# Optimization experiments

Measured on AMD Instinct MI355X. Metric: run time of the kernel, lower is better.

The kernel has to match this reference:

```python
import jax, jax.numpy as jnp
import numpy as np

N_NODES = 10000
N_EDGES = 160000
D_IN = 512
D_OUT = 512


def setup_inputs() -> dict:
    key = jax.random.key(0)
    k_x, k_e, k_wl, k_wr = jax.random.split(key, 4)
    x = jax.random.normal(k_x, (N_NODES, D_IN), dtype=jnp.float32)
    edge_index = jax.random.randint(k_e, (2, N_EDGES), 0, N_NODES, dtype=jnp.int64)
    scale = 1.0 / np.sqrt(D_IN)
    W_l = jax.random.normal(k_wl, (D_IN, D_OUT), dtype=jnp.float32) * scale
    W_r = jax.random.normal(k_wr, (D_IN, D_OUT), dtype=jnp.float32) * scale
    b = jnp.zeros((D_OUT,), dtype=jnp.float32)
    return {"x": x, "edge_index": edge_index, "W_l": W_l, "W_r": W_r, "b": b}


def reference(x, edge_index, W_l, W_r, b):
    # dropout p=0.0 -> identity
    src = edge_index[0]  # message sources (x_j)
    dst = edge_index[1]  # aggregation targets (i)
    n = x.shape[0]
    # mean neighbor aggregation: scatter-add messages, divide by in-degree
    msg = x[src]                                   # [E, D_in]
    agg = jax.ops.segment_sum(msg, dst, num_segments=n)        # [N, D_in]
    deg = jax.ops.segment_sum(jnp.ones((src.shape[0],), x.dtype), dst, num_segments=n)
    mean = agg / jnp.maximum(deg, 1.0)[:, None]
    # SAGEConv: lin_l(aggregated) + lin_r(root), bias in lin_l
    h = mean @ W_l + b + x @ W_r                   # [N, D_out]
    # Swish activation
    return h * jax.nn.sigmoid(h)
```

## Files before the change

kernel.cpp:

```cpp
#include <hip/hip_runtime.h>
#include <cstdint>
#include <cstddef>

typedef unsigned short ushort_t;
typedef __attribute__((ext_vector_type(8))) short short8;
typedef __attribute__((ext_vector_type(4))) float float4_;
typedef __attribute__((ext_vector_type(2))) float float2_;

#define GLOBAL_AS __attribute__((address_space(1)))
#define LDS_AS    __attribute__((address_space(3)))

#define D_FEAT 512
#define KDIM   1024
#define CAP    80
#define BK     128

__device__ __forceinline__ ushort_t f2bf(float f) {
    union { float f; unsigned int i; } v; v.f = f;
    unsigned int x = v.i;
    unsigned int r = (x + 0x7fffu + ((x >> 16) & 1u)) >> 16;
    return (ushort_t)r;
}

__device__ __forceinline__ void accq(float* acc, uint2 v) {
    float2_ a01 = __builtin_amdgcn_cvt_pk_f32_fp8(v.x, false);
    float2_ a23 = __builtin_amdgcn_cvt_pk_f32_fp8(v.x, true);
    float2_ a45 = __builtin_amdgcn_cvt_pk_f32_fp8(v.y, false);
    float2_ a67 = __builtin_amdgcn_cvt_pk_f32_fp8(v.y, true);
    acc[0] += a01.x; acc[1] += a01.y;
    acc[2] += a23.x; acc[3] += a23.y;
    acc[4] += a45.x; acc[5] += a45.y;
    acc[6] += a67.x; acc[7] += a67.y;
}

__global__ __launch_bounds__(256) void prep_kernel(
    const float* __restrict__ Wl, const float* __restrict__ Wr,
    const float* __restrict__ x, const int* __restrict__ ei,
    ushort_t* __restrict__ BT, ushort_t* __restrict__ xb,
    unsigned char* __restrict__ xq, unsigned int* __restrict__ cnt,
    int* __restrict__ colbuf, int N, int E, int nchunks, int cb) {
    int b = blockIdx.x;
    int t = threadIdx.x;
    if (b < cb) {
        int idx = b * 256 + t;
        if (idx >= nchunks) return;
        int row = idx >> 7;
        int c = (idx & 127) << 2;
        float4 v = *(const float4*)&x[(size_t)row * D_FEAT + c];
        ushort_t o[4] = {f2bf(v.x), f2bf(v.y), f2bf(v.z), f2bf(v.w)};
        *(uint2*)&xb[(size_t)row * D_FEAT + c] = *(const uint2*)o;
        int pk = 0;
        pk = __builtin_amdgcn_cvt_pk_fp8_f32(v.x, v.y, pk, false);
        pk = __builtin_amdgcn_cvt_pk_fp8_f32(v.z, v.w, pk, true);
        *(int*)&xq[(size_t)row * D_FEAT + c] = pk;
    } else if (b < cb + 128) {
        int bb = b - cb;
        __shared__ float tile[64][68];
        int kb = (bb & 15) * 64, nb = (bb >> 4) * 64;
#pragma unroll
        for (int ph = 0; ph < 4; ++ph) {
            int f = t * 4 + ph * 1024;
            int k = f >> 6, n = f & 63;
            int gk = kb + k;
            const float* W = (gk < 512) ? (Wl + (size_t)gk * 512 + nb + n)
                                        : (Wr + (size_t)(gk - 512) * 512 + nb + n);
            *(float4*)&tile[k][n] = *(const float4*)W;
        }
        __syncthreads();
#pragma unroll
        for (int ph = 0; ph < 4; ++ph) {
            int f = t * 4 + ph * 1024;
            int n = f >> 6, k = f & 63;
            ushort_t tmp[4];
#pragma unroll
            for (int j = 0; j < 4; ++j) tmp[j] = f2bf(tile[k + j][n]);
            *(uint2*)&BT[(size_t)(nb + n) * KDIM + kb + k] = *(const uint2*)tmp;
        }
    } else {
        int e = ((b - cb - 128) * 256 + t) * 2;
        if (e >= E) return;
        unsigned int V = cnt[N];
        int2 d2 = *(const int2*)&ei[E + e];
        int2 s2 = *(const int2*)&ei[e];
        unsigned int p0 = atomicAdd(&cnt[d2.x], 1u) - V;
        if (p0 < CAP) colbuf[(size_t)d2.x * CAP + p0] = s2.x;
        if (e + 1 < E) {
            unsigned int p1 = atomicAdd(&cnt[d2.y], 1u) - V;
            if (p1 < CAP) colbuf[(size_t)d2.y * CAP + p1] = s2.y;
        }
    }
}

__global__ __launch_bounds__(256) void agg_kernel(
    const unsigned char* __restrict__ xq, ushort_t* __restrict__ mb,
    const unsigned int* __restrict__ cnt, const int* __restrict__ colbuf,
    int n) {
    int w = threadIdx.x >> 6, l = threadIdx.x & 63;
    int node = blockIdx.x * 4 + w;
    if (node >= n) return;
    unsigned int V = cnt[n];
    int f = l << 3;
    const unsigned char* gsrc = xq + f;
    const int* bucket = colbuf + (size_t)node * CAP;
    float acc[8] = {0.f, 0.f, 0.f, 0.f, 0.f, 0.f, 0.f, 0.f};
    int deg = (int)(cnt[node] - V);
    int e = deg < CAP ? deg : CAP;
    int j = 0;
    for (; j + 7 < e; j += 8) {
        int4 i0 = *(const int4*)&bucket[j];
        int4 i1 = *(const int4*)&bucket[j + 4];
        uint2 v0 = *(const uint2*)(gsrc + (size_t)i0.x * D_FEAT);
        uint2 v1 = *(const uint2*)(gsrc + (size_t)i0.y * D_FEAT);
        uint2 v2 = *(const uint2*)(gsrc + (size_t)i0.z * D_FEAT);
        uint2 v3 = *(const uint2*)(gsrc + (size_t)i0.w * D_FEAT);
        uint2 v4 = *(const uint2*)(gsrc + (size_t)i1.x * D_FEAT);
        uint2 v5 = *(const uint2*)(gsrc + (size_t)i1.y * D_FEAT);
        uint2 v6 = *(const uint2*)(gsrc + (size_t)i1.z * D_FEAT);
        uint2 v7 = *(const uint2*)(gsrc + (size_t)i1.w * D_FEAT);
        accq(acc, v0); accq(acc, v1); accq(acc, v2); accq(acc, v3);
        accq(acc, v4); accq(acc, v5); accq(acc, v6); accq(acc, v7);
    }
    if (j + 3 < e) {
        int4 i0 = *(const int4*)&bucket[j];
        uint2 v0 = *(const uint2*)(gsrc + (size_t)i0.x * D_FEAT);
        uint2 v1 = *(const uint2*)(gsrc + (size_t)i0.y * D_FEAT);
        uint2 v2 = *(const uint2*)(gsrc + (size_t)i0.z * D_FEAT);
        uint2 v3 = *(const uint2*)(gsrc + (size_t)i0.w * D_FEAT);
        accq(acc, v0); accq(acc, v1); accq(acc, v2); accq(acc, v3);
        j += 4;
    }
    for (; j < e; ++j) {
        uint2 v0 = *(const uint2*)(gsrc + (size_t)bucket[j] * D_FEAT);
        accq(acc, v0);
    }
    float scale = 1.0f / (float)(deg > 1 ? deg : 1);
    ushort_t o[8];
#pragma unroll
    for (int k = 0; k < 8; ++k) o[k] = f2bf(acc[k] * scale);
    *(uint4*)&mb[(size_t)node * D_FEAT + f] = *(const uint4*)o;
}

__global__ __launch_bounds__(256) void gemm_kernel(
    const ushort_t* __restrict__ mb, const ushort_t* __restrict__ xb,
    const ushort_t* __restrict__ BT, const float* __restrict__ bias,
    float* __restrict__ out, int nrows) {
    __shared__ ushort_t As[64 * BK];
    __shared__ ushort_t Bs[64 * BK];
    int b = blockIdx.x;
    int sg = b >> 6, local = b & 63;
    int tile_m = (sg * 8 + (local & 7)) * 64;
    int tile_n = (local >> 3) * 64;
    int tid = threadIdx.x;
    int l = tid & 63;
    int w = tid >> 6;
    int lm = l & 15, q = l >> 4;
    int wm = (w >> 1) * 32, wn = (w & 1) * 32;

    float4_ acc[2][2];
#pragma unroll
    for (int i = 0; i < 2; ++i)
#pragma unroll
        for (int j = 0; j < 2; ++j) acc[i][j] = (float4_)(0.f);

    for (int k0 = 0; k0 < KDIM; k0 += BK) {
        const ushort_t* Asrc = (k0 < 512) ? mb : xb;
        int kk = k0 & 511;
#pragma unroll
        for (int cc = 0; cc < 4; ++cc) {
            int c = tid + cc * 256;
            int row = c >> 4;
            int kc = (c & 15) ^ (row & 15);
            const ushort_t* gp =
                Asrc + (size_t)(tile_m + row) * D_FEAT + kk + kc * 8;
            __builtin_amdgcn_global_load_lds(
                (const GLOBAL_AS unsigned int*)gp,
                (LDS_AS unsigned int*)&As[c * 8], 16, 0, 0);
            const ushort_t* gq =
                BT + (size_t)(tile_n + row) * KDIM + k0 + kc * 8;
            __builtin_amdgcn_global_load_lds(
                (const GLOBAL_AS unsigned int*)gq,
                (LDS_AS unsigned int*)&Bs[c * 8], 16, 0, 0);
        }
        __syncthreads();

#pragma unroll
        for (int s = 0; s < 4; ++s) {
            int kc = s * 4 + q;
            short8 a[2], bb[2];
#pragma unroll
            for (int i = 0; i < 2; ++i) {
                int row = wm + i * 16 + lm;
                a[i] = *(const short8*)&As[row * BK + ((kc ^ (row & 15)) << 3)];
            }
#pragma unroll
            for (int j = 0; j < 2; ++j) {
                int col = wn + j * 16 + lm;
                bb[j] = *(const short8*)&Bs[col * BK + ((kc ^ (col & 15)) << 3)];
            }
#pragma unroll
            for (int i = 0; i < 2; ++i)
#pragma unroll
                for (int j = 0; j < 2; ++j)
                    acc[i][j] = __builtin_amdgcn_mfma_f32_16x16x32_bf16(
                        a[i], bb[j], acc[i][j], 0, 0, 0);
        }
        __syncthreads();
    }

#pragma unroll
    for (int j = 0; j < 2; ++j) {
        int gcol = tile_n + wn + j * 16 + lm;
        float bv = bias[gcol];
#pragma unroll
        for (int i = 0; i < 2; ++i) {
#pragma unroll
            for (int r = 0; r < 4; ++r) {
                int grow = tile_m + wm + i * 16 + q * 4 + r;
                if (grow < nrows) {
                    float h = acc[i][j][r] + bv;
                    float sw = h / (1.f + __expf(-h));
                    out[(size_t)grow * D_FEAT + gcol] = sw;
                }
            }
        }
    }
}

extern "C" void kernel_launch(void* const* d_in, const int* in_sizes, int n_in,
                              void* d_out, int out_size, void* d_ws, size_t ws_size,
                              hipStream_t stream) {
    const float* x    = (const float*)d_in[0];
    const int*   ei   = (const int*)d_in[1];
    const float* Wl   = (const float*)d_in[2];
    const float* Wr   = (const float*)d_in[3];
    const float* bias = (const float*)d_in[4];
    float* out = (float*)d_out;

    const int N = in_sizes[0] / D_FEAT;
    const int E = in_sizes[1] / 2;
    int mt = (N + 63) / 64;
    mt = (mt + 7) & ~7;
    const int M_PAD = mt * 64;

    char* ws = (char*)d_ws;
    size_t off = 0;
    auto take = [&](size_t bytes) -> char* {
        char* p = ws + off;
        off += (bytes + 255) & ~(size_t)255;
        return p;
    };
    ushort_t*      xb     = (ushort_t*)take((size_t)M_PAD * D_FEAT * 2);
    ushort_t*      mb     = (ushort_t*)take((size_t)M_PAD * D_FEAT * 2);
    ushort_t*      BT     = (ushort_t*)take((size_t)D_FEAT * KDIM * 2);
    unsigned char* xq     = (unsigned char*)take((size_t)M_PAD * D_FEAT);
    unsigned int*  cnt    = (unsigned int*)take((size_t)M_PAD * 4);
    int*           colbuf = (int*)take((size_t)M_PAD * CAP * 4);

    int nchunks = N * (D_FEAT / 4);
    int cb = (nchunks + 255) / 256;
    int eb = (E / 2 + 255) / 256;
    prep_kernel<<<cb + 128 + eb, 256, 0, stream>>>(
        Wl, Wr, x, ei, BT, xb, xq, cnt, colbuf, N, E, nchunks, cb);

    agg_kernel<<<(N + 3) / 4, 256, 0, stream>>>(xq, mb, cnt, colbuf, N);

    gemm_kernel<<<mt * 8, 256, 0, stream>>>(mb, xb, BT, bias, out, N);
}
```

Measured before the change: 127.8 us.

## Enlarge GEMM tiles to 128x128 with 4x4 MFMA per wave and XCD-aware mapping

The GEMM block tile grows from 64x64 to 128x128, with each wave computing a 64x64 sub-tile (4x4 MFMAs) and the K step halved to 64 so shared memory stays the same size. Block indices are remapped so that consecutive blocks on the same XCD share M rows across the four N tiles, which should improve L2 reuse. The larger tiles raise arithmetic intensity and cut redundant global loads of A and B. In exchange the grid shrinks to about 320 blocks, register use per thread goes up, and there are twice as many sync iterations.

Result: slower. 139.1 us (+8.8%).

```diff
diff --git a/kernel.cpp b/kernel.cpp
--- a/kernel.cpp
+++ b/kernel.cpp
@@ -13,7 +13,7 @@
 #define D_FEAT 512
 #define KDIM   1024
 #define CAP    80
-#define BK     128
+#define BK     64
 
 __device__ __forceinline__ ushort_t f2bf(float f) {
     union { float f; unsigned int i; } v; v.f = f;
@@ -143,24 +143,24 @@
 __global__ __launch_bounds__(256) void gemm_kernel(
     const ushort_t* __restrict__ mb, const ushort_t* __restrict__ xb,
     const ushort_t* __restrict__ BT, const float* __restrict__ bias,
-    float* __restrict__ out, int nrows) {
-    __shared__ ushort_t As[64 * BK];
-    __shared__ ushort_t Bs[64 * BK];
+    float* __restrict__ out, int nrows, int mpx) {
+    __shared__ ushort_t As[128 * BK];
+    __shared__ ushort_t Bs[128 * BK];
     int b = blockIdx.x;
-    int sg = b >> 6, local = b & 63;
-    int tile_m = (sg * 8 + (local & 7)) * 64;
-    int tile_n = (local >> 3) * 64;
+    int xcd = b & 7, j = b >> 3;
+    int tile_m = (xcd * mpx + (j >> 2)) * 128;
+    int tile_n = (j & 3) * 128;
     int tid = threadIdx.x;
     int l = tid & 63;
     int w = tid >> 6;
     int lm = l & 15, q = l >> 4;
-    int wm = (w >> 1) * 32, wn = (w & 1) * 32;
-
-    float4_ acc[2][2];
-#pragma unroll
-    for (int i = 0; i < 2; ++i)
-#pragma unroll
-        for (int j = 0; j < 2; ++j) acc[i][j] = (float4_)(0.f);
+    int wm = (w >> 1) * 64, wn = (w & 1) * 64;
+
+    float4_ acc[4][4];
+#pragma unroll
+    for (int i = 0; i < 4; ++i)
+#pragma unroll
+        for (int jj = 0; jj < 4; ++jj) acc[i][jj] = (float4_)(0.f);
 
     for (int k0 = 0; k0 < KDIM; k0 += BK) {
         const ushort_t* Asrc = (k0 < 512) ? mb : xb;
@@ -168,8 +168,8 @@
 #pragma unroll
         for (int cc = 0; cc < 4; ++cc) {
             int c = tid + cc * 256;
-            int row = c >> 4;
-            int kc = (c & 15) ^ (row & 15);
+            int row = c >> 3;
+            int kc = (c & 7) ^ (row & 7);
             const ushort_t* gp =
                 Asrc + (size_t)(tile_m + row) * D_FEAT + kk + kc * 8;
             __builtin_amdgcn_global_load_lds(
@@ -184,40 +184,40 @@
         __syncthreads();
 
 #pragma unroll
-        for (int s = 0; s < 4; ++s) {
+        for (int s = 0; s < 2; ++s) {
             int kc = s * 4 + q;
-            short8 a[2], bb[2];
-#pragma unroll
-            for (int i = 0; i < 2; ++i) {
+            short8 a[4], bb[4];
+#pragma unroll
+            for (int i = 0; i < 4; ++i) {
                 int row = wm + i * 16 + lm;
-                a[i] = *(const short8*)&As[row * BK + ((kc ^ (row & 15)) << 3)];
+                a[i] = *(const short8*)&As[row * BK + ((kc ^ (row & 7)) << 3)];
             }
 #pragma unroll
-            for (int j = 0; j < 2; ++j) {
-                int col = wn + j * 16 + lm;
-                bb[j] = *(const short8*)&Bs[col * BK + ((kc ^ (col & 15)) << 3)];
+            for (int jj = 0; jj < 4; ++jj) {
+                int col = wn + jj * 16 + lm;
+                bb[jj] = *(const short8*)&Bs[col * BK + ((kc ^ (col & 7)) << 3)];
             }
 #pragma unroll
-            for (int i = 0; i < 2; ++i)
-#pragma unroll
-                for (int j = 0; j < 2; ++j)
-                    acc[i][j] = __builtin_amdgcn_mfma_f32_16x16x32_bf16(
-                        a[i], bb[j], acc[i][j], 0, 0, 0);
+            for (int i = 0; i < 4; ++i)
+#pragma unroll
+                for (int jj = 0; jj < 4; ++jj)
+                    acc[i][jj] = __builtin_amdgcn_mfma_f32_16x16x32_bf16(
+                        a[i], bb[jj], acc[i][jj], 0, 0, 0);
         }
         __syncthreads();
     }
 
 #pragma unroll
-    for (int j = 0; j < 2; ++j) {
-        int gcol = tile_n + wn + j * 16 + lm;
+    for (int jj = 0; jj < 4; ++jj) {
+        int gcol = tile_n + wn + jj * 16 + lm;
         float bv = bias[gcol];
 #pragma unroll
-        for (int i = 0; i < 2; ++i) {
+        for (int i = 0; i < 4; ++i) {
 #pragma unroll
             for (int r = 0; r < 4; ++r) {
                 int grow = tile_m + wm + i * 16 + q * 4 + r;
                 if (grow < nrows) {
-                    float h = acc[i][j][r] + bv;
+                    float h = acc[i][jj][r] + bv;
                     float sw = h / (1.f + __expf(-h));
                     out[(size_t)grow * D_FEAT + gcol] = sw;
                 }
@@ -238,9 +238,10 @@
 
     const int N = in_sizes[0] / D_FEAT;
     const int E = in_sizes[1] / 2;
-    int mt = (N + 63) / 64;
+    int mt = (N + 127) / 128;
     mt = (mt + 7) & ~7;
-    const int M_PAD = mt * 64;
+    const int M_PAD = mt * 128;
+    const int mpx = mt / 8;
 
     char* ws = (char*)d_ws;
     size_t off = 0;
@@ -264,5 +265,5 @@
 
     agg_kernel<<<(N + 3) / 4, 256, 0, stream>>>(xq, mb, cnt, colbuf, N);
 
-    gemm_kernel<<<mt * 8, 256, 0, stream>>>(mb, xb, BT, bias, out, N);
-}
+    gemm_kernel<<<mt * 4, 256, 0, stream>>>(mb, xb, BT, bias, out, N, mpx);
+}
```
